# Kernel tuning notes

Measured on AMD Instinct MI355X. Metric: run time of the kernel, lower is better.

## Reference

```python
import jax, jax.numpy as jnp
import numpy as np

# dims: N batch, O out_channels, CI in_channels, H=W vertices, R rank
N, O, CI, H, R = 8, 32, 16, 512, 8


def setup_inputs() -> dict:
    key = jax.random.key(0)
    kx, kw, kb = jax.random.split(key, 3)
    X = jax.random.normal(kx, (N, CI, H, H), dtype=jnp.float32)
    # learnable left generator (right generator aliases it under symmetry=True)
    weight_L = jax.random.normal(kw, (O, CI, H, R), dtype=jnp.float32) * 0.02
    fan_in = CI * H * R  # torch fan_in for a (O, CI, H, R) weight
    bound = 1.0 / np.sqrt(fan_in)
    bias = jax.random.uniform(kb, (O,), dtype=jnp.float32, minval=-bound, maxval=bound)
    # coupling='split': fixed (non-learnable) +/-1 diagonal coupling, first O//2 channels negative
    coupling = jnp.ones((O, CI, R, 1), dtype=jnp.float32).at[: O // 2].multiply(-1.0)
    return {"X": X, "weight_L": weight_L, "bias": bias, "coupling": coupling}


def reference(X, weight_L, bias, coupling):
    # --- template expansion: T[o,c] = L diag(coupling) L^T  (symmetric, low-rank) ---
    # coupling: (O,CI,R,1) -> per-rank sign broadcast over the rank axis of L
    Lc = weight_L * coupling[..., 0][..., None, :]            # (O,CI,H,R)
    T = jnp.einsum('ochr,ocwr->ochw', Lc, weight_L)           # (O,CI,H,W)
    # --- crosshair similarity, with the in_channel sum pulled inside ---
    P = jnp.einsum('nchw,ochw->nohw', X, T)                   # (N,O,H,W)
    out = P.sum(-1, keepdims=True) + P.sum(-2, keepdims=True) - P
    out = out + bias[None, :, None, None]
    # --- delete diagonal ---
    eye = jnp.eye(out.shape[-1], dtype=out.dtype)
    return out * (1.0 - eye)
```

## Files before the change

kernel.cpp:

```cpp
#include <hip/hip_runtime.h>
#include <cstdint>
#include <cstddef>

#define Ndim 8
#define Odim 32
#define Cdim 16
#define Hdim 512
#define Rdim 8
#define TW 64
#define TH 4
#define NBW (Hdim/TW)
#define NBH (Hdim/TH)

typedef _Float16 half2_t __attribute__((ext_vector_type(2)));

union U16 { uint4 u; half2_t h[4]; _Float16 f[8]; };

__device__ __forceinline__ half2_t pk(float a, float b) {
    half2_t h; h[0] = (_Float16)a; h[1] = (_Float16)b; return h;
}

#if defined(__has_builtin)
#if __has_builtin(__builtin_amdgcn_fdot2)
#define HAVE_FDOT2 1
#endif
#endif

__device__ __forceinline__ float fdot2f(half2_t a, half2_t b, float acc) {
#ifdef HAVE_FDOT2
    return __builtin_amdgcn_fdot2(a, b, acc, false);
#else
    return acc + (float)a[0] * (float)b[0] + (float)a[1] * (float)b[1];
#endif
}

__device__ __forceinline__ void stage16(const uint4* g, uint4* l) {
    __builtin_amdgcn_global_load_lds(
        (const __attribute__((address_space(1))) uint32_t*)g,
        (__attribute__((address_space(3))) uint32_t*)l, 16, 0, 0);
}

template<int CTRL>
__device__ __forceinline__ float dppadd(float v) {
    return v + __int_as_float(__builtin_amdgcn_update_dpp(
        0, __float_as_int(v), CTRL, 0xf, 0xf, true));
}
__device__ __forceinline__ float wave_sum63(float v) {
    v = dppadd<0xB1>(v);
    v = dppadd<0x4E>(v);
    v = dppadd<0x141>(v);
    v = dppadd<0x140>(v);
    v = dppadd<0x142>(v);
    v = dppadd<0x143>(v);
    return v;
}

__global__ __launch_bounds__(256)
void sylo_prep(const float* __restrict__ L, const float* __restrict__ coup,
               uint4* __restrict__ lsigT, uint4* __restrict__ lraw)
{
    int row = blockIdx.x * 256 + threadIdx.x;
    int oc = row >> 9, h = row & 511;
    int o = oc >> 4, c = oc & 15;
    const float4* lp = (const float4*)(L + (size_t)row * Rdim);
    const float4* cp = (const float4*)(coup + (size_t)oc * Rdim);
    float4 l0 = lp[0], l1 = lp[1];
    float4 c0 = cp[0], c1 = cp[1];
    U16 s, r;
    s.h[0] = pk(l0.x * c0.x, l0.y * c0.y); s.h[1] = pk(l0.z * c0.z, l0.w * c0.w);
    s.h[2] = pk(l1.x * c1.x, l1.y * c1.y); s.h[3] = pk(l1.z * c1.z, l1.w * c1.w);
    r.h[0] = pk(l0.x, l0.y); r.h[1] = pk(l0.z, l0.w);
    r.h[2] = pk(l1.x, l1.y); r.h[3] = pk(l1.z, l1.w);
    lsigT[((size_t)o * Hdim + h) * Cdim + c] = s.u;
    lraw[row] = r.u;
}

template<int PASS, int MODE>
__global__ __launch_bounds__(256, 4)
void sylo_main(const float* __restrict__ Xg, const float* __restrict__ Lg,
               const float* __restrict__ coupg, const float* __restrict__ biasg,
               const uint4* __restrict__ lsigT, const uint4* __restrict__ lraw,
               float* __restrict__ outg,
               float* __restrict__ rsp, float* __restrict__ csp,
               float* __restrict__ rs, float* __restrict__ cs)
{
    const int tid = threadIdx.x;
    const int j = tid & 63, iw = tid >> 6;
    const int bw = blockIdx.x, bh = blockIdx.y;
    const int w0 = bw * TW, h0 = bh * TH;
    const int hh = h0 + iw;
    const int ww = w0 + j;
    const size_t S = (size_t)Ndim * Odim * Hdim;

    __shared__ __align__(16) uint4 lw[2][Cdim][TW];
    __shared__ float csl[TH][Ndim][TW];

    half2_t xa[64];
    {
        const size_t HH = (size_t)Hdim * Hdim;
        const size_t q = (size_t)hh * Hdim + ww;
        #pragma unroll
        for (int c = 0; c < Cdim; c += 2) {
            #pragma unroll
            for (int n = 0; n < Ndim; ++n)
                xa[(c >> 1) * 8 + n] = pk(Xg[(size_t)(n * Cdim + c) * HH + q],
                                          Xg[(size_t)(n * Cdim + c + 1) * HH + q]);
        }
    }

    const int ruh = __builtin_amdgcn_readfirstlane(hh);

    if (MODE < 2) {
        #pragma unroll
        for (int k = 0; k < 4; ++k) {
            int c = iw * 4 + k;
            stage16(lraw + ((size_t)c * Hdim + w0 + j), &lw[0][c][0]);
        }
    }

    for (int o = 0; o < Odim; ++o) {
        const int cur = o & 1;
        __syncthreads();

        if (MODE < 2) {
            if (o + 1 < Odim) {
                #pragma unroll
                for (int k = 0; k < 4; ++k) {
                    int c = iw * 4 + k;
                    stage16(lraw + ((size_t)((o + 1) * Cdim + c) * Hdim + w0 + j),
                            &lw[cur ^ 1][c][0]);
                }
            }
        } else {
            #pragma unroll
            for (int k = 0; k < 4; ++k) {
                int e = tid + k * 256, c = e >> 6, w = e & 63;
                const float4* gp = (const float4*)(Lg + ((size_t)(o * Cdim + c) * Hdim + w0 + w) * Rdim);
                float4 l0 = gp[0], l1 = gp[1];
                U16 t;
                t.h[0] = pk(l0.x, l0.y); t.h[1] = pk(l0.z, l0.w);
                t.h[2] = pk(l1.x, l1.y); t.h[3] = pk(l1.z, l1.w);
                lw[0][c][w] = t.u;
            }
            __syncthreads();
        }

        half2_t t2[8];
        float tprev = 0.f;
        #pragma unroll
        for (int c = 0; c < Cdim; ++c) {
            U16 A, B;
            if (MODE < 2) {
                A.u = lsigT[((size_t)o * Hdim + ruh) * Cdim + c];
            } else {
                const float4* a0 = (const float4*)(Lg + ((size_t)(o * Cdim + c) * Hdim + ruh) * Rdim);
                const float4* cpp = (const float4*)(coupg + (size_t)(o * Cdim + c) * Rdim);
                float4 l0 = a0[0], l1 = a0[1];
                float4 c0 = cpp[0], c1 = cpp[1];
                A.h[0] = pk(l0.x * c0.x, l0.y * c0.y); A.h[1] = pk(l0.z * c0.z, l0.w * c0.w);
                A.h[2] = pk(l1.x * c1.x, l1.y * c1.y); A.h[3] = pk(l1.z * c1.z, l1.w * c1.w);
            }
            B.u = lw[MODE < 2 ? cur : 0][c][j];
            float t = 0.f;
            #pragma unroll
            for (int r = 0; r < 4; ++r) t = fdot2f(A.h[r], B.h[r], t);
            if (c & 1) t2[c >> 1] = pk(tprev, t);
            else       tprev = t;
        }

        float p[Ndim];
        #pragma unroll
        for (int n = 0; n < Ndim; ++n) p[n] = 0.f;
        #pragma unroll
        for (int cp8 = 0; cp8 < 8; ++cp8) {
            #pragma unroll
            for (int n = 0; n < Ndim; ++n)
                p[n] = fdot2f(t2[cp8], xa[cp8 * 8 + n], p[n]);
        }

        if (PASS == 0) {
            #pragma unroll
            for (int n = 0; n < Ndim; ++n) {
                float r = wave_sum63(p[n]);
                if (j == 63) {
                    size_t i0 = (size_t)(n * Odim + o) * Hdim + hh;
                    if (MODE == 0) rsp[(size_t)bw * S + i0] = r;
                    else atomicAdd(&rs[i0], r);
                }
                csl[iw][n][j] = p[n];
            }
            __syncthreads();
            #pragma unroll
            for (int k = 0; k < 2; ++k) {
                int e = tid + k * 256;
                int n = e >> 6, jj = e & 63;
                float v = csl[0][n][jj] + csl[1][n][jj] + csl[2][n][jj] + csl[3][n][jj];
                size_t idx = (size_t)(n * Odim + o) * Hdim + w0 + jj;
                if (MODE == 0) csp[(size_t)bh * S + idx] = v;
                else atomicAdd(&cs[idx], v);
            }
        } else {
            float bb = biasg[o];
            #pragma unroll
            for (int n = 0; n < Ndim; ++n) {
                size_t i0 = (size_t)(n * Odim + o) * Hdim;
                float rv = rs[i0 + (size_t)ruh];
                float cv = cs[i0 + ww];
                float v = rv + cv - p[n] + bb;
                if (hh == ww) v = 0.f;
                outg[(i0 + hh) * Hdim + ww] = v;
            }
        }
    }
}

__global__ __launch_bounds__(256)
void sylo_reduce(const float* __restrict__ rsp, const float* __restrict__ csp,
                 float* __restrict__ rs, float* __restrict__ cs)
{
    int t = blockIdx.x * 256 + threadIdx.x;
    const size_t S = (size_t)Ndim * Odim * Hdim;
    float a = 0.f;
    #pragma unroll
    for (int k = 0; k < NBW; ++k) a += rsp[(size_t)k * S + t];
    rs[t] = a;
    float b = 0.f;
    #pragma unroll 16
    for (int k = 0; k < NBH; ++k) b += csp[(size_t)k * S + t];
    cs[t] = b;
}

extern "C" void kernel_launch(void* const* d_in, const int* in_sizes, int n_in,
                              void* d_out, int out_size, void* d_ws, size_t ws_size,
                              hipStream_t stream)
{
    const float* X    = (const float*)d_in[0];
    const float* L    = (const float*)d_in[1];
    const float* bias = (const float*)d_in[2];
    const float* coup = (const float*)d_in[3];
    float* out = (float*)d_out;

    const size_t S    = (size_t)Ndim * Odim * Hdim;
    const size_t NL16 = (size_t)Odim * Cdim * Hdim;
    const size_t need0 = NL16 * 16 * 2 + (NBW + NBH + 2) * S * 4;
    const size_t need1 = NL16 * 16 * 2 + 2 * S * 4;
    dim3 grid(NBW, NBH), blk(256);

    if (ws_size >= need0) {
        uint4* lsigT = (uint4*)d_ws;
        uint4* lraw  = lsigT + NL16;
        float* rsp = (float*)(lraw + NL16);
        float* csp = rsp + (size_t)NBW * S;
        float* rs  = csp + (size_t)NBH * S;
        float* cs  = rs + S;
        sylo_prep<<<dim3(1024), blk, 0, stream>>>(L, coup, lsigT, lraw);
        sylo_main<0,0><<<grid, blk, 0, stream>>>(X, L, coup, bias, lsigT, lraw, out, rsp, csp, rs, cs);
        sylo_reduce<<<dim3(512), blk, 0, stream>>>(rsp, csp, rs, cs);
        sylo_main<1,0><<<grid, blk, 0, stream>>>(X, L, coup, bias, lsigT, lraw, out, rsp, csp, rs, cs);
    } else if (ws_size >= need1) {
        uint4* lsigT = (uint4*)d_ws;
        uint4* lraw  = lsigT + NL16;
        float* rs = (float*)(lraw + NL16);
        float* cs = rs + S;
        hipMemsetAsync(rs, 0, 2 * S * sizeof(float), stream);
        sylo_prep<<<dim3(1024), blk, 0, stream>>>(L, coup, lsigT, lraw);
        sylo_main<0,1><<<grid, blk, 0, stream>>>(X, L, coup, bias, lsigT, lraw, out, nullptr, nullptr, rs, cs);
        sylo_main<1,1><<<grid, blk, 0, stream>>>(X, L, coup, bias, lsigT, lraw, out, nullptr, nullptr, rs, cs);
    } else {
        float* rs = (float*)d_ws;
        float* cs = rs + S;
        hipMemsetAsync(rs, 0, 2 * S * sizeof(float), stream);
        sylo_main<0,2><<<grid, blk, 0, stream>>>(X, L, coup, bias, nullptr, nullptr, out, nullptr, nullptr, rs, cs);
        sylo_main<1,2><<<grid, blk, 0, stream>>>(X, L, coup, bias, nullptr, nullptr, out, nullptr, nullptr, rs, cs);
    }
}
```

Baseline: 285.7 us.

## Drop LDS staging of L and batch column sums via LDS atomics

The right-factor L rows are now read straight from global memory (cached) instead of being double-buffered in LDS through global_load_lds. This removes the per-output-channel barrier. Column partial sums are accumulated with LDS atomics into a buffer covering 16 output channels, and are flushed only every 16 channels, cutting barriers from two per channel to two per 16. The costs are LDS atomic contention across the four waves, a larger LDS footprint, and redundant global/L1 loads of L per lane.

```diff
diff --git a/kernel.cpp b/kernel.cpp
--- a/kernel.cpp
+++ b/kernel.cpp
@@ -11,6 +11,7 @@
 #define TH 4
 #define NBW (Hdim/TW)
 #define NBH (Hdim/TH)
+#define OCH 16
 
 typedef _Float16 half2_t __attribute__((ext_vector_type(2)));
 
@@ -32,12 +33,6 @@
 #else
     return acc + (float)a[0] * (float)b[0] + (float)a[1] * (float)b[1];
 #endif
-}
-
-__device__ __forceinline__ void stage16(const uint4* g, uint4* l) {
-    __builtin_amdgcn_global_load_lds(
-        (const __attribute__((address_space(1))) uint32_t*)g,
-        (__attribute__((address_space(3))) uint32_t*)l, 16, 0, 0);
 }
 
 template<int CTRL>
@@ -92,8 +87,7 @@
     const int ww = w0 + j;
     const size_t S = (size_t)Ndim * Odim * Hdim;
 
-    __shared__ __align__(16) uint4 lw[2][Cdim][TW];
-    __shared__ float csl[TH][Ndim][TW];
+    __shared__ float csa[Ndim][OCH][TW];
 
     half2_t xa[64];
     {
@@ -110,41 +104,14 @@
 
     const int ruh = __builtin_amdgcn_readfirstlane(hh);
 
-    if (MODE < 2) {
-        #pragma unroll
-        for (int k = 0; k < 4; ++k) {
-            int c = iw * 4 + k;
-            stage16(lraw + ((size_t)c * Hdim + w0 + j), &lw[0][c][0]);
-        }
+    if (PASS == 0) {
+        #pragma unroll
+        for (int k = 0; k < Ndim * OCH * TW / 256; ++k)
+            ((float*)csa)[tid + k * 256] = 0.f;
+        __syncthreads();
     }
 
     for (int o = 0; o < Odim; ++o) {
-        const int cur = o & 1;
-        __syncthreads();
-
-        if (MODE < 2) {
-            if (o + 1 < Odim) {
-                #pragma unroll
-                for (int k = 0; k < 4; ++k) {
-                    int c = iw * 4 + k;
-                    stage16(lraw + ((size_t)((o + 1) * Cdim + c) * Hdim + w0 + j),
-                            &lw[cur ^ 1][c][0]);
-                }
-            }
-        } else {
-            #pragma unroll
-            for (int k = 0; k < 4; ++k) {
-                int e = tid + k * 256, c = e >> 6, w = e & 63;
-                const float4* gp = (const float4*)(Lg + ((size_t)(o * Cdim + c) * Hdim + w0 + w) * Rdim);
-                float4 l0 = gp[0], l1 = gp[1];
-                U16 t;
-                t.h[0] = pk(l0.x, l0.y); t.h[1] = pk(l0.z, l0.w);
-                t.h[2] = pk(l1.x, l1.y); t.h[3] = pk(l1.z, l1.w);
-                lw[0][c][w] = t.u;
-            }
-            __syncthreads();
-        }
-
         half2_t t2[8];
         float tprev = 0.f;
         #pragma unroll
@@ -152,15 +119,19 @@
             U16 A, B;
             if (MODE < 2) {
                 A.u = lsigT[((size_t)o * Hdim + ruh) * Cdim + c];
+                B.u = lraw[(size_t)(o * Cdim + c) * Hdim + ww];
             } else {
                 const float4* a0 = (const float4*)(Lg + ((size_t)(o * Cdim + c) * Hdim + ruh) * Rdim);
+                const float4* b0 = (const float4*)(Lg + ((size_t)(o * Cdim + c) * Hdim + ww) * Rdim);
                 const float4* cpp = (const float4*)(coupg + (size_t)(o * Cdim + c) * Rdim);
                 float4 l0 = a0[0], l1 = a0[1];
+                float4 m0 = b0[0], m1 = b0[1];
                 float4 c0 = cpp[0], c1 = cpp[1];
                 A.h[0] = pk(l0.x * c0.x, l0.y * c0.y); A.h[1] = pk(l0.z * c0.z, l0.w * c0.w);
                 A.h[2] = pk(l1.x * c1.x, l1.y * c1.y); A.h[3] = pk(l1.z * c1.z, l1.w * c1.w);
-            }
-            B.u = lw[MODE < 2 ? cur : 0][c][j];
+                B.h[0] = pk(m0.x, m0.y); B.h[1] = pk(m0.z, m0.w);
+                B.h[2] = pk(m1.x, m1.y); B.h[3] = pk(m1.z, m1.w);
+            }
             float t = 0.f;
             #pragma unroll
             for (int r = 0; r < 4; ++r) t = fdot2f(A.h[r], B.h[r], t);
@@ -179,6 +150,7 @@
         }
 
         if (PASS == 0) {
+            const int oc = o & (OCH - 1);
             #pragma unroll
             for (int n = 0; n < Ndim; ++n) {
                 float r = wave_sum63(p[n]);
@@ -187,17 +159,22 @@
                     if (MODE == 0) rsp[(size_t)bw * S + i0] = r;
                     else atomicAdd(&rs[i0], r);
                 }
-                csl[iw][n][j] = p[n];
-            }
-            __syncthreads();
-            #pragma unroll
-            for (int k = 0; k < 2; ++k) {
-                int e = tid + k * 256;
-                int n = e >> 6, jj = e & 63;
-                float v = csl[0][n][jj] + csl[1][n][jj] + csl[2][n][jj] + csl[3][n][jj];
-                size_t idx = (size_t)(n * Odim + o) * Hdim + w0 + jj;
-                if (MODE == 0) csp[(size_t)bh * S + idx] = v;
-                else atomicAdd(&cs[idx], v);
+                atomicAdd(&csa[n][oc][j], p[n]);
+            }
+            if (oc == OCH - 1) {
+                const int base = o - (OCH - 1);
+                __syncthreads();
+                #pragma unroll
+                for (int k = 0; k < Ndim * OCH * TW / 256; ++k) {
+                    int f = tid + k * 256;
+                    int n = f >> 10, oo = (f >> 6) & (OCH - 1), jj = f & 63;
+                    float v = ((float*)csa)[f];
+                    ((float*)csa)[f] = 0.f;
+                    size_t idx = (size_t)(n * Odim + base + oo) * Hdim + w0 + jj;
+                    if (MODE == 0) csp[(size_t)bh * S + idx] = v;
+                    else atomicAdd(&cs[idx], v);
+                }
+                __syncthreads();
             }
         } else {
             float bb = biasg[o];
```

New measurement: 616.0 us. +115.6%, slower.

## Batch column-sum flushes across output channels and relax per-channel barriers

Applied to the files above, without the earlier changes.

Column partial sums now accumulate in LDS via shared-memory atomics across 8 output channels and are flushed together, so the per-channel __syncthreads and global writes happen once every 8 channels instead of every channel. The per-iteration barrier is replaced by a manual vmcnt wait plus s_barrier at the loop end, letting the async LDS prefetch overlap compute. X is held as per-batch f16x16 vectors, and launch bounds drop to 3 waves per EU to allow more registers. The costs are LDS atomic contention, a larger LDS footprint, and possibly lower occupancy. The hand-counted vmcnt(8) could also be wrong if the compiler emits a different number of outstanding loads.

```diff
diff --git a/kernel.cpp b/kernel.cpp
--- a/kernel.cpp
+++ b/kernel.cpp
@@ -11,10 +11,12 @@
 #define TH 4
 #define NBW (Hdim/TW)
 #define NBH (Hdim/TH)
+#define OCH 8
 
 typedef _Float16 half2_t __attribute__((ext_vector_type(2)));
-
-union U16 { uint4 u; half2_t h[4]; _Float16 f[8]; };
+typedef _Float16 f16x16 __attribute__((ext_vector_type(16)));
+
+union U16 { uint4 u; half2_t h[4]; };
 
 __device__ __forceinline__ half2_t pk(float a, float b) {
     half2_t h; h[0] = (_Float16)a; h[1] = (_Float16)b; return h;
@@ -32,6 +34,10 @@
 #else
     return acc + (float)a[0] * (float)b[0] + (float)a[1] * (float)b[1];
 #endif
+}
+
+__device__ __forceinline__ half2_t h2pair(f16x16 v, int cp) {
+    half2_t r; r[0] = v[2 * cp]; r[1] = v[2 * cp + 1]; return r;
 }
 
 __device__ __forceinline__ void stage16(const uint4* g, uint4* l) {
@@ -75,8 +81,10 @@
     lraw[row] = r.u;
 }
 
+#define FORN(op) op(0) op(1) op(2) op(3) op(4) op(5) op(6) op(7)
+
 template<int PASS, int MODE>
-__global__ __launch_bounds__(256, 4)
+__global__ __launch_bounds__(256, 3)
 void sylo_main(const float* __restrict__ Xg, const float* __restrict__ Lg,
                const float* __restrict__ coupg, const float* __restrict__ biasg,
                const uint4* __restrict__ lsigT, const uint4* __restrict__ lraw,
@@ -93,22 +101,24 @@
     const size_t S = (size_t)Ndim * Odim * Hdim;
 
     __shared__ __align__(16) uint4 lw[2][Cdim][TW];
-    __shared__ float csl[TH][Ndim][TW];
-
-    half2_t xa[64];
-    {
-        const size_t HH = (size_t)Hdim * Hdim;
-        const size_t q = (size_t)hh * Hdim + ww;
-        #pragma unroll
-        for (int c = 0; c < Cdim; c += 2) {
-            #pragma unroll
-            for (int n = 0; n < Ndim; ++n)
-                xa[(c >> 1) * 8 + n] = pk(Xg[(size_t)(n * Cdim + c) * HH + q],
-                                          Xg[(size_t)(n * Cdim + c + 1) * HH + q]);
-        }
-    }
+    __shared__ float csa[(PASS == 0) ? (Ndim * OCH * TW) : 64];
+
+    const size_t HH = (size_t)Hdim * Hdim;
+    const size_t q = (size_t)hh * Hdim + ww;
+#define XDECL(n) f16x16 xv##n;
+    FORN(XDECL)
+#define XLOAD(n) { const float* xp = Xg + (size_t)(n) * Cdim * HH + q;          \
+    _Pragma("unroll") for (int c = 0; c < Cdim; ++c)                            \
+        xv##n[c] = (_Float16)xp[(size_t)c * HH]; }
+    FORN(XLOAD)
 
     const int ruh = __builtin_amdgcn_readfirstlane(hh);
+
+    if (PASS == 0) {
+        #pragma unroll
+        for (int k = 0; k < Ndim * OCH * TW / 256; ++k)
+            csa[tid + k * 256] = 0.f;
+    }
 
     if (MODE < 2) {
         #pragma unroll
@@ -117,10 +127,10 @@
             stage16(lraw + ((size_t)c * Hdim + w0 + j), &lw[0][c][0]);
         }
     }
+    __syncthreads();
 
     for (int o = 0; o < Odim; ++o) {
         const int cur = o & 1;
-        __syncthreads();
 
         if (MODE < 2) {
             if (o + 1 < Odim) {
@@ -132,6 +142,7 @@
                 }
             }
         } else {
+            __syncthreads();
             #pragma unroll
             for (int k = 0; k < 4; ++k) {
                 int e = tid + k * 256, c = e >> 6, w = e & 63;
@@ -172,13 +183,13 @@
         #pragma unroll
         for (int n = 0; n < Ndim; ++n) p[n] = 0.f;
         #pragma unroll
-        for (int cp8 = 0; cp8 < 8; ++cp8) {
-            #pragma unroll
-            for (int n = 0; n < Ndim; ++n)
-                p[n] = fdot2f(t2[cp8], xa[cp8 * 8 + n], p[n]);
+        for (int cp = 0; cp < 8; ++cp) {
+#define XP(n) p[n] = fdot2f(t2[cp], h2pair(xv##n, cp), p[n]);
+            FORN(XP)
         }
 
         if (PASS == 0) {
+            const int oc = o & (OCH - 1);
             #pragma unroll
             for (int n = 0; n < Ndim; ++n) {
                 float r = wave_sum63(p[n]);
@@ -187,17 +198,22 @@
                     if (MODE == 0) rsp[(size_t)bw * S + i0] = r;
                     else atomicAdd(&rs[i0], r);
                 }
-                csl[iw][n][j] = p[n];
-            }
-            __syncthreads();
-            #pragma unroll
-            for (int k = 0; k < 2; ++k) {
-                int e = tid + k * 256;
-                int n = e >> 6, jj = e & 63;
-                float v = csl[0][n][jj] + csl[1][n][jj] + csl[2][n][jj] + csl[3][n][jj];
-                size_t idx = (size_t)(n * Odim + o) * Hdim + w0 + jj;
-                if (MODE == 0) csp[(size_t)bh * S + idx] = v;
-                else atomicAdd(&cs[idx], v);
+                atomicAdd(&csa[(n * OCH + oc) * TW + j], p[n]);
+            }
+            if (oc == OCH - 1) {
+                const int base = o - (OCH - 1);
+                __syncthreads();
+                #pragma unroll
+                for (int k = 0; k < Ndim * OCH * TW / 256; ++k) {
+                    int f = tid + k * 256;
+                    int n = f >> 9, oo = (f >> 6) & (OCH - 1), jj = f & 63;
+                    float v = csa[f];
+                    csa[f] = 0.f;
+                    size_t idx = (size_t)(n * Odim + base + oo) * Hdim + w0 + jj;
+                    if (MODE == 0) csp[(size_t)bh * S + idx] = v;
+                    else atomicAdd(&cs[idx], v);
+                }
+                __syncthreads();
             }
         } else {
             float bb = biasg[o];
@@ -210,6 +226,11 @@
                 if (hh == ww) v = 0.f;
                 outg[(i0 + hh) * Hdim + ww] = v;
             }
+        }
+
+        if (MODE < 2) {
+            asm volatile("s_waitcnt vmcnt(8)" ::: "memory");
+            __builtin_amdgcn_s_barrier();
         }
     }
 }
```

After: 687.8 us. +140.8%, slower.

## Batch column-sum reduction across channel pairs and use explicit vmcnt barriers

Applied to the files above, without the earlier changes.

Replaces __syncthreads around the double-buffered lraw staging with raw s_barrier plus targeted s_waitcnt vmcnt counts. Outstanding stores and prefetches can then stay in flight across iterations instead of draining at every barrier. The column-sum shared reduction is now done once per pair of output channels using a doubled csl buffer, which halves the barriers in pass 0. It also lowers the launch-bounds occupancy hint from 4 to 3 and uses template unrolling. The hand-tuned vmcnt counts are fragile: if the compiler emits a different number of memory ops, the code could race.

```diff
diff --git a/kernel.cpp b/kernel.cpp
--- a/kernel.cpp
+++ b/kernel.cpp
@@ -1,6 +1,7 @@
 #include <hip/hip_runtime.h>
 #include <cstdint>
 #include <cstddef>
+#include <utility>
 
 #define Ndim 8
 #define Odim 32
@@ -14,7 +15,16 @@
 
 typedef _Float16 half2_t __attribute__((ext_vector_type(2)));
 
-union U16 { uint4 u; half2_t h[4]; _Float16 f[8]; };
+union U16 { uint4 u; half2_t h[4]; };
+
+template <class F, int... Is>
+__device__ __forceinline__ void unroll_impl(F&& f, std::integer_sequence<int, Is...>) {
+    (f(std::integral_constant<int, Is>{}), ...);
+}
+template <int N, class F>
+__device__ __forceinline__ void unrollN(F&& f) {
+    unroll_impl(static_cast<F&&>(f), std::make_integer_sequence<int, N>{});
+}
 
 __device__ __forceinline__ half2_t pk(float a, float b) {
     half2_t h; h[0] = (_Float16)a; h[1] = (_Float16)b; return h;
@@ -76,7 +86,7 @@
 }
 
 template<int PASS, int MODE>
-__global__ __launch_bounds__(256, 4)
+__global__ __launch_bounds__(256, 3)
 void sylo_main(const float* __restrict__ Xg, const float* __restrict__ Lg,
                const float* __restrict__ coupg, const float* __restrict__ biasg,
                const uint4* __restrict__ lsigT, const uint4* __restrict__ lraw,
@@ -93,47 +103,51 @@
     const size_t S = (size_t)Ndim * Odim * Hdim;
 
     __shared__ __align__(16) uint4 lw[2][Cdim][TW];
-    __shared__ float csl[TH][Ndim][TW];
+    __shared__ float csl[(PASS == 0) ? (2 * TH * Ndim * TW) : 64];
 
     half2_t xa[64];
     {
         const size_t HH = (size_t)Hdim * Hdim;
         const size_t q = (size_t)hh * Hdim + ww;
-        #pragma unroll
-        for (int c = 0; c < Cdim; c += 2) {
-            #pragma unroll
-            for (int n = 0; n < Ndim; ++n)
-                xa[(c >> 1) * 8 + n] = pk(Xg[(size_t)(n * Cdim + c) * HH + q],
-                                          Xg[(size_t)(n * Cdim + c + 1) * HH + q]);
-        }
+        unrollN<8>([&](auto cpi) {
+            unrollN<8>([&](auto ni) {
+                constexpr int cp = decltype(cpi)::value, n = decltype(ni)::value;
+                xa[cp * 8 + n] = pk(Xg[(size_t)(n * Cdim + 2 * cp) * HH + q],
+                                    Xg[(size_t)(n * Cdim + 2 * cp + 1) * HH + q]);
+            });
+        });
     }
 
     const int ruh = __builtin_amdgcn_readfirstlane(hh);
 
     if (MODE < 2) {
-        #pragma unroll
-        for (int k = 0; k < 4; ++k) {
+        unrollN<4>([&](auto ki) {
+            constexpr int k = decltype(ki)::value;
             int c = iw * 4 + k;
             stage16(lraw + ((size_t)c * Hdim + w0 + j), &lw[0][c][0]);
-        }
+        });
+        asm volatile("s_waitcnt vmcnt(0)" ::: "memory");
+        __builtin_amdgcn_s_barrier();
+        __builtin_amdgcn_sched_barrier(0);
     }
 
     for (int o = 0; o < Odim; ++o) {
-        const int cur = o & 1;
-        __syncthreads();
+        const int cur = (MODE < 2) ? (o & 1) : 0;
 
         if (MODE < 2) {
             if (o + 1 < Odim) {
-                #pragma unroll
-                for (int k = 0; k < 4; ++k) {
+                unrollN<4>([&](auto ki) {
+                    constexpr int k = decltype(ki)::value;
                     int c = iw * 4 + k;
                     stage16(lraw + ((size_t)((o + 1) * Cdim + c) * Hdim + w0 + j),
                             &lw[cur ^ 1][c][0]);
-                }
+                });
             }
+            __builtin_amdgcn_sched_barrier(0);
         } else {
-            #pragma unroll
-            for (int k = 0; k < 4; ++k) {
+            __syncthreads();
+            unrollN<4>([&](auto ki) {
+                constexpr int k = decltype(ki)::value;
                 int e = tid + k * 256, c = e >> 6, w = e & 63;
                 const float4* gp = (const float4*)(Lg + ((size_t)(o * Cdim + c) * Hdim + w0 + w) * Rdim);
                 float4 l0 = gp[0], l1 = gp[1];
@@ -141,14 +155,14 @@
                 t.h[0] = pk(l0.x, l0.y); t.h[1] = pk(l0.z, l0.w);
                 t.h[2] = pk(l1.x, l1.y); t.h[3] = pk(l1.z, l1.w);
                 lw[0][c][w] = t.u;
-            }
+            });
             __syncthreads();
         }
 
         half2_t t2[8];
         float tprev = 0.f;
-        #pragma unroll
-        for (int c = 0; c < Cdim; ++c) {
+        unrollN<16>([&](auto ci) {
+            constexpr int c = decltype(ci)::value;
             U16 A, B;
             if (MODE < 2) {
                 A.u = lsigT[((size_t)o * Hdim + ruh) * Cdim + c];
@@ -160,56 +174,80 @@
                 A.h[0] = pk(l0.x * c0.x, l0.y * c0.y); A.h[1] = pk(l0.z * c0.z, l0.w * c0.w);
                 A.h[2] = pk(l1.x * c1.x, l1.y * c1.y); A.h[3] = pk(l1.z * c1.z, l1.w * c1.w);
             }
-            B.u = lw[MODE < 2 ? cur : 0][c][j];
+            B.u = lw[cur][c][j];
             float t = 0.f;
-            #pragma unroll
-            for (int r = 0; r < 4; ++r) t = fdot2f(A.h[r], B.h[r], t);
-            if (c & 1) t2[c >> 1] = pk(tprev, t);
-            else       tprev = t;
-        }
+            unrollN<4>([&](auto ri) {
+                constexpr int r = decltype(ri)::value;
+                t = fdot2f(A.h[r], B.h[r], t);
+            });
+            if constexpr (c & 1) t2[c >> 1] = pk(tprev, t);
+            else                 tprev = t;
+        });
 
         float p[Ndim];
-        #pragma unroll
-        for (int n = 0; n < Ndim; ++n) p[n] = 0.f;
-        #pragma unroll
-        for (int cp8 = 0; cp8 < 8; ++cp8) {
-            #pragma unroll
-            for (int n = 0; n < Ndim; ++n)
-                p[n] = fdot2f(t2[cp8], xa[cp8 * 8 + n], p[n]);
-        }
+        unrollN<8>([&](auto ni) { p[decltype(ni)::value] = 0.f; });
+        unrollN<8>([&](auto cpi) {
+            unrollN<8>([&](auto ni) {
+                constexpr int cp = decltype(cpi)::value, n = decltype(ni)::value;
+                p[n] = fdot2f(t2[cp], xa[cp * 8 + n], p[n]);
+            });
+        });
 
         if (PASS == 0) {
-            #pragma unroll
-            for (int n = 0; n < Ndim; ++n) {
+            const int oc = o & 1;
+            unrollN<8>([&](auto ni) {
+                constexpr int n = decltype(ni)::value;
                 float r = wave_sum63(p[n]);
                 if (j == 63) {
                     size_t i0 = (size_t)(n * Odim + o) * Hdim + hh;
                     if (MODE == 0) rsp[(size_t)bw * S + i0] = r;
                     else atomicAdd(&rs[i0], r);
                 }
-                csl[iw][n][j] = p[n];
-            }
-            __syncthreads();
-            #pragma unroll
-            for (int k = 0; k < 2; ++k) {
-                int e = tid + k * 256;
-                int n = e >> 6, jj = e & 63;
-                float v = csl[0][n][jj] + csl[1][n][jj] + csl[2][n][jj] + csl[3][n][jj];
-                size_t idx = (size_t)(n * Odim + o) * Hdim + w0 + jj;
-                if (MODE == 0) csp[(size_t)bh * S + idx] = v;
-                else atomicAdd(&cs[idx], v);
+                csl[((oc * TH + iw) * Ndim + n) * TW + j] = p[n];
+            });
+            if (oc == 1) {
+                if (MODE < 2) {
+                    asm volatile("s_waitcnt lgkmcnt(0)" ::: "memory");
+                    __builtin_amdgcn_s_barrier();
+                    __builtin_amdgcn_sched_barrier(0);
+                } else __syncthreads();
+                unrollN<4>([&](auto ki) {
+                    constexpr int k = decltype(ki)::value;
+                    int f = tid + k * 256;
+                    int oo = f >> 9, n = (f >> 6) & 7, jj = f & 63;
+                    float v = csl[((oo * TH + 0) * Ndim + n) * TW + jj]
+                            + csl[((oo * TH + 1) * Ndim + n) * TW + jj]
+                            + csl[((oo * TH + 2) * Ndim + n) * TW + jj]
+                            + csl[((oo * TH + 3) * Ndim + n) * TW + jj];
+                    size_t idx = (size_t)(n * Odim + (o - 1 + oo)) * Hdim + w0 + jj;
+                    if (MODE == 0) csp[(size_t)bh * S + idx] = v;
+                    else atomicAdd(&cs[idx], v);
+                });
+                if (MODE < 2) __builtin_amdgcn_s_barrier();
+                else          __syncthreads();
             }
         } else {
             float bb = biasg[o];
-            #pragma unroll
-            for (int n = 0; n < Ndim; ++n) {
+            unrollN<8>([&](auto ni) {
+                constexpr int n = decltype(ni)::value;
                 size_t i0 = (size_t)(n * Odim + o) * Hdim;
                 float rv = rs[i0 + (size_t)ruh];
                 float cv = cs[i0 + ww];
                 float v = rv + cv - p[n] + bb;
                 if (hh == ww) v = 0.f;
                 outg[(i0 + hh) * Hdim + ww] = v;
+            });
+        }
+
+        if (MODE < 2) {
+            if (PASS == 0) {
+                if ((o & 1) == 1) asm volatile("s_waitcnt vmcnt(12)" ::: "memory");
+                else              asm volatile("s_waitcnt vmcnt(8)"  ::: "memory");
+            } else {
+                asm volatile("s_waitcnt vmcnt(16)" ::: "memory");
             }
+            __builtin_amdgcn_s_barrier();
+            __builtin_amdgcn_sched_barrier(0);
         }
     }
 }
```

After: 312.8 us. 9.5% more time.
